# Kernel tuning notes

Hardware: AMD Instinct MI355X
Metric: run time of the kernel (lower is better)

Reference implementation:

```python
import jax, jax.numpy as jnp
import numpy as np

N, E, F, ED, L = 50000, 800000, 64, 16, 2
EPS_BN = 1e-5


def setup_inputs() -> dict:
    key = jax.random.key(0)
    ks = jax.random.split(key, 8)
    s = 0.05
    return {
        "x": jax.random.normal(ks[0], (N, F), jnp.float32),
        "edge_index": jax.random.randint(ks[1], (2, E), 0, N),
        "edge_attr": jax.random.normal(ks[2], (E, ED), jnp.float32),
        # per-layer stacked params (L layers)
        "We": jax.random.normal(ks[3], (L, ED, F), jnp.float32) * s,
        "be": jnp.zeros((L, F), jnp.float32),
        "Wpre": jax.random.normal(ks[4], (L, 2 * F, F), jnp.float32) * s,
        "bpre": jnp.zeros((L, F), jnp.float32),
        "Wpost": jax.random.normal(ks[5], (L, 7 * F, F), jnp.float32) * s,
        "bpost": jnp.zeros((L, F), jnp.float32),
        "Wlin": jax.random.normal(ks[6], (L, F, F), jnp.float32) * s,
        "blin": jnp.zeros((L, F), jnp.float32),
        "gamma": jnp.ones((L, F), jnp.float32),
        "beta": jnp.zeros((L, F), jnp.float32),
    }


def _layer(x, src, dst, edge_attr, We, be, Wpre, bpre, Wpost, bpost, Wlin, blin, gamma, beta):
    # message: edge encoder + pre-MLP on cat(x_j, e)   [E, F]
    e = edge_attr @ We + be
    h = jnp.concatenate([x[src], e], axis=-1) @ Wpre + bpre
    # multi-aggregator segment reduce to target nodes (index = dst)
    cnt = jax.ops.segment_sum(jnp.ones(h.shape[0], h.dtype), dst, num_segments=N)
    safe_cnt = jnp.maximum(cnt, 1.0)
    mean = jax.ops.segment_sum(h, dst, num_segments=N) / safe_cnt[:, None]
    empty = (cnt == 0)[:, None]
    mn = jnp.where(empty, 0.0, jax.ops.segment_min(h, dst, num_segments=N))
    mx = jnp.where(empty, 0.0, jax.ops.segment_max(h, dst, num_segments=N))
    agg = jnp.concatenate([mean, mn, mx], axis=-1)  # [N, 3F]
    # scalers: identity, then amplification (deg=None => avg from bincount of degrees)
    deg_i = cnt.astype(jnp.int32)
    bc = jnp.bincount(deg_i, length=N).astype(h.dtype)
    avg_log = jnp.mean(jnp.log(bc + 1.0))
    amp = (jnp.log(safe_cnt + 1.0) / avg_log)[:, None]
    out = jnp.concatenate([agg, agg * amp], axis=-1)  # [N, 6F]
    # post-MLP on cat(x, aggregated), final linear
    out = jnp.concatenate([x, out], axis=-1) @ Wpost + bpost  # [N, F]
    out = out @ Wlin + blin
    # BatchNorm1d (batch stats, biased var) + ReLU
    mu = out.mean(axis=0)
    var = jnp.mean((out - mu) ** 2, axis=0)
    out = gamma * (out - mu) / jnp.sqrt(var + EPS_BN) + beta
    return jax.nn.relu(out)


def reference(x, edge_index, edge_attr, We, be, Wpre, bpre, Wpost, bpost, Wlin, blin, gamma, beta):
    src, dst = edge_index[0], edge_index[1]
    for l in range(L):
        x = _layer(x, src, dst, edge_attr, We[l], be[l], Wpre[l], bpre[l],
                   Wpost[l], bpost[l], Wlin[l], blin[l], gamma[l], beta[l])
    return x
```

## Files before the change

### kernel.cpp

```cpp
#include <hip/hip_runtime.h>
#include <math.h>

static constexpr int NN = 50000;
static constexpr long NE = 800000;
static constexpr int FF = 64;
static constexpr int EDIM = 16;
static constexpr int NLAYER = 2;
static constexpr float EPSBN = 1e-5f;
static constexpr int NGRP = NN / 16;
static constexpr int SCB = 512;
static constexpr int NSCB = (NN + SCB - 1) / SCB;

typedef __attribute__((ext_vector_type(8))) short short8v;
typedef __attribute__((ext_vector_type(4))) float f32x4;

#define MFMA16(a, b, c) __builtin_amdgcn_mfma_f32_16x16x32_bf16(a, b, c, 0, 0, 0)

__device__ __forceinline__ short f2bf(float f) {
    unsigned u = __float_as_uint(f);
    unsigned r = u + 0x7FFFu + ((u >> 16) & 1u);
    return (short)(r >> 16);
}
__device__ __forceinline__ float bf2f(unsigned short h) {
    return __uint_as_float(((unsigned)h) << 16);
}
__device__ __forceinline__ unsigned pk2(float lo, float hi) {
    return (unsigned)(unsigned short)f2bf(lo) | ((unsigned)(unsigned short)f2bf(hi) << 16);
}
__device__ __forceinline__ short8v pack8(const float* p) {
    const float4* q = (const float4*)p;
    float4 a = q[0], b = q[1];
    short8v v;
    v[0] = f2bf(a.x); v[1] = f2bf(a.y); v[2] = f2bf(a.z); v[3] = f2bf(a.w);
    v[4] = f2bf(b.x); v[5] = f2bf(b.y); v[6] = f2bf(b.z); v[7] = f2bf(b.w);
    return v;
}
__device__ __forceinline__ void pack8s(const float* p, short8v& hi, short8v& lo) {
    const float4* q = (const float4*)p;
    float4 a = q[0], b = q[1];
    float v[8] = {a.x, a.y, a.z, a.w, b.x, b.y, b.z, b.w};
#pragma unroll
    for (int j = 0; j < 8; ++j) {
        short h = f2bf(v[j]);
        hi[j] = h;
        lo[j] = f2bf(v[j] - bf2f((unsigned short)h));
    }
}
__device__ __forceinline__ void pack8fs(const float* v, short8v& hi, short8v& lo) {
#pragma unroll
    for (int j = 0; j < 8; ++j) {
        short h = f2bf(v[j]);
        hi[j] = h;
        lo[j] = f2bf(v[j] - bf2f((unsigned short)h));
    }
}

__global__ void fold_kernel(const float* __restrict__ We, const float* __restrict__ be,
                            const float* __restrict__ Wpre, const float* __restrict__ bpre,
                            const float* __restrict__ Wpost, const float* __restrict__ bpost,
                            const float* __restrict__ Wlin, const float* __restrict__ blin,
                            float* __restrict__ Weff, float* __restrict__ beff,
                            float* __restrict__ Wc, float* __restrict__ cfold) {
    int l = blockIdx.x >> 4;
    int s = blockIdx.x & 15;
    int t = threadIdx.x;
    const float* We_l    = We    + l * EDIM * FF;
    const float* Wpre_e  = Wpre  + l * 2 * FF * FF + FF * FF;
    const float* Wpost_l = Wpost + l * 7 * FF * FF;
    const float* Wlin_l  = Wlin  + l * FF * FF;

    __shared__ float slin[FF * FF];
    __shared__ float spre[FF * FF];
    for (int i = t; i < FF * FF; i += blockDim.x) { slin[i] = Wlin_l[i]; spre[i] = Wpre_e[i]; }
    __syncthreads();

    for (int i = s * 256 + t; i < EDIM * FF; i += 16 * 256) {
        int j = i >> 6, f = i & 63;
        float a = 0.f;
        for (int k = 0; k < FF; ++k) a += We_l[j * FF + k] * spre[k * FF + f];
        Weff[l * EDIM * FF + i] = a;
    }
    for (int i = s * 256 + t; i < FF; i += 16 * 256) {
        float a = bpre[l * FF + i];
        for (int k = 0; k < FF; ++k) a += be[l * FF + k] * spre[k * FF + i];
        beff[l * FF + i] = a;
    }
    for (int i = s * 256 + t; i < 7 * FF * FF; i += 16 * 256) {
        int r = i >> 6, f = i & 63;
        float a = 0.f;
        for (int k = 0; k < FF; ++k) a += Wpost_l[r * FF + k] * slin[k * FF + f];
        Wc[l * 7 * FF * FF + i] = a;
    }
    for (int i = s * 256 + t; i < FF; i += 16 * 256) {
        float a = blin[l * FF + i];
        for (int k = 0; k < FF; ++k) a += bpost[l * FF + k] * slin[k * FF + i];
        cfold[l * FF + i] = a;
    }
}

__global__ void fragify_all(const float* __restrict__ Wpre, const float* __restrict__ Weff,
                            const float* __restrict__ Wc,
                            short* __restrict__ WpreF, short* __restrict__ WeffF,
                            short* __restrict__ WcFh, short* __restrict__ WcFl) {
    int b = blockIdx.x;
    int l = b / 17, r = b % 17;
    int t = threadIdx.x;
    const float* src; short* dh; short* dl = nullptr; int kc, Kreal;
    if (r < 2)      { src = Wpre + (size_t)l * 2 * FF * FF; dh = WpreF + l * 4096;  kc = r;     Kreal = 64; }
    else if (r < 3) { src = Weff + (size_t)l * EDIM * FF;   dh = WeffF + l * 2048;  kc = 0;     Kreal = 16; }
    else            { src = Wc   + (size_t)l * 7 * FF * FF; dh = WcFh + l * 28672;
                      dl = WcFl + l * 28672;                                        kc = r - 3; Kreal = 448; }
    int idx = kc * 256 + t;
    int lane = idx & 63, nt = (idx >> 6) & 3;
    int m = lane & 15, kh = lane >> 4;
    short8v hv, lv;
#pragma unroll
    for (int j = 0; j < 8; ++j) {
        int k = kc * 32 + kh * 8 + j;
        float val = (k < Kreal) ? src[k * FF + nt * 16 + m] : 0.f;
        short h = f2bf(val);
        hv[j] = h;
        lv[j] = f2bf(val - bf2f((unsigned short)h));
    }
    ((short8v*)dh)[idx] = hv;
    if (dl) ((short8v*)dl)[idx] = lv;
}


__global__ void build_zero(int* __restrict__ rowcnt, int* __restrict__ fill,
                           int* __restrict__ bc, float* __restrict__ avglog) {
    long i = (long)blockIdx.x * 256 + threadIdx.x;
    long stride = (long)gridDim.x * 256;
    for (long j = i; j < NN; j += stride) { rowcnt[j] = 0; fill[j] = 0; bc[j] = 0; }
    if (i == 0) avglog[0] = 0.f;
}

__global__ void hist_dst(const int* __restrict__ ei, int* __restrict__ rowcnt) {
    long e = (long)blockIdx.x * 256 + threadIdx.x;
    if (e < NE) atomicAdd(&rowcnt[ei[NE + e]], 1);
}

__global__ void scan_a(const int* __restrict__ rowcnt, int* __restrict__ part) {
    __shared__ int red[SCB];
    int t = threadIdx.x;
    int i = blockIdx.x * SCB + t;
    red[t] = (i < NN) ? rowcnt[i] : 0;
    __syncthreads();
    for (int o = SCB / 2; o > 0; o >>= 1) {
        if (t < o) red[t] += red[t + o];
        __syncthreads();
    }
    if (t == 0) part[blockIdx.x] = red[0];
}

__global__ void scan_b(int* __restrict__ part, int* __restrict__ rowptr) {
    __shared__ int s[128];
    int t = threadIdx.x;
    int v = (t < NSCB) ? part[t] : 0;
    s[t] = v;
    __syncthreads();
    for (int o = 1; o < 128; o <<= 1) {
        int u = (t >= o) ? s[t - o] : 0;
        __syncthreads();
        s[t] += u;
        __syncthreads();
    }
    if (t < NSCB) part[t] = s[t] - v;
    if (t == 127) rowptr[NN] = s[127];
}

__global__ void scan_c(const int* __restrict__ rowcnt, const int* __restrict__ part,
                       int* __restrict__ rowptr) {
    __shared__ int s[SCB];
    int t = threadIdx.x;
    int i = blockIdx.x * SCB + t;
    int v = (i < NN) ? rowcnt[i] : 0;
    s[t] = v;
    __syncthreads();
    for (int o = 1; o < SCB; o <<= 1) {
        int u = (t >= o) ? s[t - o] : 0;
        __syncthreads();
        s[t] += u;
        __syncthreads();
    }
    if (i < NN) rowptr[i] = part[blockIdx.x] + s[t] - v;
}

__global__ void scatter2(const int* __restrict__ ei, const float* __restrict__ attr,
                         const int* __restrict__ rowptr, int* __restrict__ fill,
                         int* __restrict__ srcp, short* __restrict__ attrb) {
    long e = (long)blockIdx.x * 256 + threadIdx.x;
    if (e >= NE) return;
    int d = ei[NE + e];
    int p = rowptr[d] + atomicAdd(&fill[d], 1);
    srcp[p] = ei[e];
    const float4* a4 = (const float4*)(attr + e * EDIM);
    float4 A = a4[0], B = a4[1], C = a4[2], D = a4[3];
    uint4 w0, w1;
    w0.x = pk2(A.x, A.y); w0.y = pk2(A.z, A.w); w0.z = pk2(B.x, B.y); w0.w = pk2(B.z, B.w);
    w1.x = pk2(C.x, C.y); w1.y = pk2(C.z, C.w); w1.z = pk2(D.x, D.y); w1.w = pk2(D.z, D.w);
    uint4* dst = (uint4*)(attrb + (long)p * EDIM);
    dst[0] = w0; dst[1] = w1;
}

__global__ void degbc2(const int* __restrict__ rowcnt, int* __restrict__ bc) {
    __shared__ int h[256];
    int t = threadIdx.x;
    h[t] = 0;
    __syncthreads();
    for (long n = (long)blockIdx.x * 256 + t; n < NN; n += (long)gridDim.x * 256) {
        int d = rowcnt[n];
        if (d < 256) {
            atomicAdd(&h[d], 1);
        } else {
            if (d >= NN) d = NN - 1;
            atomicAdd(&bc[d], 1);
        }
    }
    __syncthreads();
    int v = h[t];
    if (v) atomicAdd(&bc[t], v);
}

__global__ void avglog_kernel(const int* __restrict__ bc, float* __restrict__ total) {
    float s = 0.f;
    for (long i = (long)blockIdx.x * 256 + threadIdx.x; i < NN; i += (long)gridDim.x * 256)
        s += logf((float)bc[i] + 1.f);
    for (int o = 32; o; o >>= 1) s += __shfl_down(s, o, 64);
    __shared__ float wsum[4];
    int lane = threadIdx.x & 63, wid = threadIdx.x >> 6;
    if (lane == 0) wsum[wid] = s;
    __syncthreads();
    if (threadIdx.x == 0) atomicAdd(total, wsum[0] + wsum[1] + wsum[2] + wsum[3]);
}

__global__ void amp_kernel(const int* __restrict__ cnt, const float* __restrict__ total,
                           float* __restrict__ amp) {
    long n = (long)blockIdx.x * 256 + threadIdx.x;
    if (n < NN) {
        float avg = total[0] / (float)NN;
        float sc = fmaxf((float)cnt[n], 1.f);
        amp[n] = logf(sc + 1.f) / avg;
    }
}


__global__ __launch_bounds__(256) void xp_mfma(const float* __restrict__ xin,
                                               const short* __restrict__ WF,
                                               short* __restrict__ xpb,
                                               float* __restrict__ bnsum,
                                               float* __restrict__ bnsum2) {
    int t = threadIdx.x;
    if (blockIdx.x == 0 && t < FF) { bnsum[t] = 0.f; bnsum2[t] = 0.f; }
    int g = blockIdx.x * 4 + (t >> 6);
    if (g >= NGRP) return;
    int lane = t & 63, m = lane & 15, kh = lane >> 4;
    const float* xr = xin + (long)(g * 16 + m) * FF;
    short8v a0 = pack8(xr + kh * 8);
    short8v a1 = pack8(xr + 32 + kh * 8);
    const short8v* BF = (const short8v*)WF;
    f32x4 acc[4];
#pragma unroll
    for (int nt = 0; nt < 4; ++nt) {
        f32x4 z = {0.f, 0.f, 0.f, 0.f};
        z = MFMA16(a0, BF[(0 * 4 + nt) * 64 + lane], z);
        z = MFMA16(a1, BF[(1 * 4 + nt) * 64 + lane], z);
        acc[nt] = z;
    }
#pragma unroll
    for (int nt = 0; nt < 4; ++nt)
#pragma unroll
        for (int r = 0; r < 4; ++r) {
            long node = g * 16 + kh * 4 + r;
            xpb[node * FF + nt * 16 + m] = f2bf(acc[nt][r]);
        }
}

__global__ __launch_bounds__(256) void ep_mfma(const short* __restrict__ attrb,
                                               const short* __restrict__ WF,
                                               const float* __restrict__ beff_l,
                                               short* __restrict__ epc, long elo) {
    int t = threadIdx.x;
    int g = blockIdx.x * 4 + (t >> 6);
    int lane = t & 63, m = lane & 15, kh = lane >> 4;
    long p0 = elo + (long)g * 16;
    short8v a;
    if (kh < 2) {
        a = *(const short8v*)(attrb + (p0 + m) * EDIM + kh * 8);
    } else {
#pragma unroll
        for (int j = 0; j < 8; ++j) a[j] = 0;
    }
    const short8v* BF = (const short8v*)WF;
    float bfv[4];
#pragma unroll
    for (int nt = 0; nt < 4; ++nt) bfv[nt] = beff_l[nt * 16 + m];
    f32x4 acc[4];
#pragma unroll
    for (int nt = 0; nt < 4; ++nt) {
        f32x4 z = {0.f, 0.f, 0.f, 0.f};
        acc[nt] = MFMA16(a, BF[nt * 64 + lane], z);
    }
#pragma unroll
    for (int nt = 0; nt < 4; ++nt)
#pragma unroll
        for (int r = 0; r < 4; ++r) {
            long rel = (long)g * 16 + kh * 4 + r;
            epc[rel * FF + nt * 16 + m] = f2bf(acc[nt][r] + bfv[nt]);
        }
}

__global__ __launch_bounds__(256) void agg_merge(
    const int* __restrict__ rowptr, const int* __restrict__ srcp,
    const short* __restrict__ xpb, const short* __restrict__ epc,
    long elo, long ehi, int first,
    float* __restrict__ sumb, float* __restrict__ mnb, float* __restrict__ mxb) {
    int t = threadIdx.x;
    int n = blockIdx.x * 4 + (t >> 6);
    if (n >= NN) return;
    int lane = t & 63;
    long r0 = rowptr[n], r1 = rowptr[n + 1];
    long lo = r0 > elo ? r0 : elo;
    long hi = r1 < ehi ? r1 : ehi;
    const float INF = __builtin_huge_valf();
    float sm = 0.f, mn = INF, mx = -INF;
    if (!first && lo >= hi) return;
    const unsigned short* xu = (const unsigned short*)xpb;
    const unsigned short* eu = (const unsigned short*)epc;
    for (long base = lo; base < hi; base += 64) {
        int cnt = (int)(((hi - base) < 64) ? (hi - base) : 64);
        int sv = srcp[base + (lane < cnt ? lane : cnt - 1)];
        long eb = base - elo;
        int j = 0;
        for (; j + 4 <= cnt; j += 4) {
            int s0 = __shfl(sv, j + 0), s1 = __shfl(sv, j + 1);
            int s2 = __shfl(sv, j + 2), s3 = __shfl(sv, j + 3);
            float x0 = bf2f(xu[(long)s0 * FF + lane]);
            float x1 = bf2f(xu[(long)s1 * FF + lane]);
            float x2 = bf2f(xu[(long)s2 * FF + lane]);
            float x3 = bf2f(xu[(long)s3 * FF + lane]);
            float e0 = bf2f(eu[(eb + j + 0) * FF + lane]);
            float e1 = bf2f(eu[(eb + j + 1) * FF + lane]);
            float e2 = bf2f(eu[(eb + j + 2) * FF + lane]);
            float e3 = bf2f(eu[(eb + j + 3) * FF + lane]);
            float h0 = x0 + e0, h1 = x1 + e1, h2 = x2 + e2, h3 = x3 + e3;
            sm += (h0 + h1) + (h2 + h3);
            mn = fminf(mn, fminf(fminf(h0, h1), fminf(h2, h3)));
            mx = fmaxf(mx, fmaxf(fmaxf(h0, h1), fmaxf(h2, h3)));
        }
        for (; j < cnt; ++j) {
            int s0 = __shfl(sv, j);
            float h = bf2f(xu[(long)s0 * FF + lane]) + bf2f(eu[(eb + j) * FF + lane]);
            sm += h;
            mn = fminf(mn, h);
            mx = fmaxf(mx, h);
        }
    }
    long o = (long)n * FF + lane;
    if (first) {
        sumb[o] = sm; mnb[o] = mn; mxb[o] = mx;
    } else {
        sumb[o] += sm;
        mnb[o] = fminf(mnb[o], mn);
        mxb[o] = fmaxf(mxb[o], mx);
    }
}

__global__ __launch_bounds__(256) void node_mfma(
    const float* __restrict__ xin, const float* __restrict__ sumb,
    const float* __restrict__ mnb, const float* __restrict__ mxb,
    const int* __restrict__ rowcnt, const float* __restrict__ amp,
    const short* __restrict__ WFh, const short* __restrict__ WFl,
    const float* __restrict__ cfold_l,
    float* __restrict__ out_pre, float* __restrict__ bnsum, float* __restrict__ bnsum2) {
    __shared__ float sS[FF], sQ[FF];
    int t = threadIdx.x;
    if (t < FF) { sS[t] = 0.f; sQ[t] = 0.f; }
    __syncthreads();
    int g = blockIdx.x * 4 + (t >> 6);
    bool act = (g < NGRP);
    int lane = t & 63, m = lane & 15, kh = lane >> 4;
    if (act) {
        long n = g * 16 + m;
        int deg = rowcnt[n];
        float inv = 1.f / fmaxf((float)deg, 1.f);
        bool has = (deg > 0);
        float av = amp[n];
        const float* xr = xin + n * FF;
        float vme[16], vmn[16], vmx[16], sc16[16];
        {
            const float4* s4a = (const float4*)(sumb + n * FF + kh * 8);
            const float4* s4b = (const float4*)(sumb + n * FF + 32 + kh * 8);
            float4 a = s4a[0], b = s4a[1], c = s4b[0], d = s4b[1];
            vme[0]=a.x*inv; vme[1]=a.y*inv; vme[2]=a.z*inv; vme[3]=a.w*inv;
            vme[4]=b.x*inv; vme[5]=b.y*inv; vme[6]=b.z*inv; vme[7]=b.w*inv;
            vme[8]=c.x*inv; vme[9]=c.y*inv; vme[10]=c.z*inv; vme[11]=c.w*inv;
            vme[12]=d.x*inv; vme[13]=d.y*inv; vme[14]=d.z*inv; vme[15]=d.w*inv;
        }
        {
            const float4* s4a = (const float4*)(mnb + n * FF + kh * 8);
            const float4* s4b = (const float4*)(mnb + n * FF + 32 + kh * 8);
            float4 a = s4a[0], b = s4a[1], c = s4b[0], d = s4b[1];
            vmn[0]=has?a.x:0.f; vmn[1]=has?a.y:0.f; vmn[2]=has?a.z:0.f; vmn[3]=has?a.w:0.f;
            vmn[4]=has?b.x:0.f; vmn[5]=has?b.y:0.f; vmn[6]=has?b.z:0.f; vmn[7]=has?b.w:0.f;
            vmn[8]=has?c.x:0.f; vmn[9]=has?c.y:0.f; vmn[10]=has?c.z:0.f; vmn[11]=has?c.w:0.f;
            vmn[12]=has?d.x:0.f; vmn[13]=has?d.y:0.f; vmn[14]=has?d.z:0.f; vmn[15]=has?d.w:0.f;
        }
        {
            const float4* s4a = (const float4*)(mxb + n * FF + kh * 8);
            const float4* s4b = (const float4*)(mxb + n * FF + 32 + kh * 8);
            float4 a = s4a[0], b = s4a[1], c = s4b[0], d = s4b[1];
            vmx[0]=has?a.x:0.f; vmx[1]=has?a.y:0.f; vmx[2]=has?a.z:0.f; vmx[3]=has?a.w:0.f;
            vmx[4]=has?b.x:0.f; vmx[5]=has?b.y:0.f; vmx[6]=has?b.z:0.f; vmx[7]=has?b.w:0.f;
            vmx[8]=has?c.x:0.f; vmx[9]=has?c.y:0.f; vmx[10]=has?c.z:0.f; vmx[11]=has?c.w:0.f;
            vmx[12]=has?d.x:0.f; vmx[13]=has?d.y:0.f; vmx[14]=has?d.z:0.f; vmx[15]=has?d.w:0.f;
        }
        const short8v* BH = (const short8v*)WFh;
        const short8v* BL = (const short8v*)WFl;
        f32x4 acc[4];
#pragma unroll
        for (int nt = 0; nt < 4; ++nt) { f32x4 z = {0.f,0.f,0.f,0.f}; acc[nt] = z; }
        short8v hv, lv;
#define DO_KC3(kc) { \
        _Pragma("unroll") for (int nt = 0; nt < 4; ++nt) { \
            acc[nt] = MFMA16(hv, BH[((kc) * 4 + nt) * 64 + lane], acc[nt]); \
            acc[nt] = MFMA16(lv, BH[((kc) * 4 + nt) * 64 + lane], acc[nt]); \
            acc[nt] = MFMA16(hv, BL[((kc) * 4 + nt) * 64 + lane], acc[nt]); } }
        pack8s(xr + kh * 8, hv, lv);        DO_KC3(0)
        pack8s(xr + 32 + kh * 8, hv, lv);   DO_KC3(1)
        pack8fs(vme + 0, hv, lv);           DO_KC3(2)
        pack8fs(vme + 8, hv, lv);           DO_KC3(3)
        pack8fs(vmn + 0, hv, lv);           DO_KC3(4)
        pack8fs(vmn + 8, hv, lv);           DO_KC3(5)
        pack8fs(vmx + 0, hv, lv);           DO_KC3(6)
        pack8fs(vmx + 8, hv, lv);           DO_KC3(7)
#pragma unroll
        for (int j = 0; j < 16; ++j) sc16[j] = vme[j] * av;
        pack8fs(sc16 + 0, hv, lv);          DO_KC3(8)
        pack8fs(sc16 + 8, hv, lv);          DO_KC3(9)
#pragma unroll
        for (int j = 0; j < 16; ++j) sc16[j] = vmn[j] * av;
        pack8fs(sc16 + 0, hv, lv);          DO_KC3(10)
        pack8fs(sc16 + 8, hv, lv);          DO_KC3(11)
#pragma unroll
        for (int j = 0; j < 16; ++j) sc16[j] = vmx[j] * av;
        pack8fs(sc16 + 0, hv, lv);          DO_KC3(12)
        pack8fs(sc16 + 8, hv, lv);          DO_KC3(13)
#undef DO_KC3
        float cfv[4];
#pragma unroll
        for (int nt = 0; nt < 4; ++nt) cfv[nt] = cfold_l[nt * 16 + m];
#pragma unroll
        for (int nt = 0; nt < 4; ++nt) {
            float ps = 0.f, pq = 0.f;
#pragma unroll
            for (int r = 0; r < 4; ++r) {
                float v = acc[nt][r] + cfv[nt];
                out_pre[(long)(g * 16 + kh * 4 + r) * FF + nt * 16 + m] = v;
                ps += v;
                pq += v * v;
            }
            atomicAdd(&sS[nt * 16 + m], ps);
            atomicAdd(&sQ[nt * 16 + m], pq);
        }
    }
    __syncthreads();
    if (t < FF) {
        atomicAdd(&bnsum[t], sS[t]);
        atomicAdd(&bnsum2[t], sQ[t]);
    }
}

__global__ void bn_apply2(const float* __restrict__ out_pre,
                          const float* __restrict__ bnsum, const float* __restrict__ bnsum2,
                          const float* __restrict__ gamma_l, const float* __restrict__ beta_l,
                          float* __restrict__ xout) {
    int f = threadIdx.x & 63;
    float mu = bnsum[f] / (float)NN;
    float var = bnsum2[f] / (float)NN - mu * mu;
    var = fmaxf(var, 0.f);
    float s = gamma_l[f] * rsqrtf(var + EPSBN);
    float o = beta_l[f] - mu * s;
    long i = (long)blockIdx.x * 256 + threadIdx.x;
    long stride = (long)gridDim.x * 256;
    for (long j = i; j < (long)NN * FF; j += stride) {
        xout[j] = fmaxf(fmaf(out_pre[j], s, o), 0.f);
    }
}

extern "C" void kernel_launch(void* const* d_in, const int* in_sizes, int n_in,
                              void* d_out, int out_size, void* d_ws, size_t ws_size,
                              hipStream_t stream) {
    const float* x0    = (const float*)d_in[0];
    const int*   ei    = (const int*)d_in[1];
    const float* attr  = (const float*)d_in[2];
    const float* We    = (const float*)d_in[3];
    const float* be    = (const float*)d_in[4];
    const float* Wpre  = (const float*)d_in[5];
    const float* bpre  = (const float*)d_in[6];
    const float* Wpost = (const float*)d_in[7];
    const float* bpost = (const float*)d_in[8];
    const float* Wlin  = (const float*)d_in[9];
    const float* blin  = (const float*)d_in[10];
    const float* gamma = (const float*)d_in[11];
    const float* beta  = (const float*)d_in[12];
    float* out = (float*)d_out;

    char* ws = (char*)d_ws;
    size_t off = 0;
    auto carve = [&](size_t bytes) -> void* {
        void* p = ws + off;
        off += (bytes + 255) & ~(size_t)255;
        return p;
    };
    const size_t NFb = (size_t)NN * FF * 4;
    float*    Weff   = (float*)carve(2 * EDIM * FF * 4);
    float*    beff   = (float*)carve(2 * FF * 4);
    float*    Wc     = (float*)carve(2 * 7 * FF * FF * 4);
    float*    cfold  = (float*)carve(2 * FF * 4);
    short*    WpreF  = (short*)carve(2 * 4096 * 2);
    short*    WeffF  = (short*)carve(2 * 2048 * 2);
    short*    WcFh   = (short*)carve(2 * 28672 * 2);
    short*    WcFl   = (short*)carve(2 * 28672 * 2);
    int*      srcp   = (int*)carve(NE * 4);
    short*    attrb  = (short*)carve((size_t)NE * EDIM * 2);
    int*      rowptr = (int*)carve((NN + 1) * 4);
    int*      rowcnt = (int*)carve(NN * 4);
    int*      fill   = (int*)carve(NN * 4);
    int*      bc     = (int*)carve(NN * 4);
    float*    amp    = (float*)carve(NN * 4);
    int*      part   = (int*)carve(NSCB * 4);
    short*    xpb    = (short*)carve((size_t)NN * FF * 2);
    float*    sumb   = (float*)carve(NFb);
    float*    mnb    = (float*)carve(NFb);
    float*    mxb    = (float*)carve(NFb);
    float*    xbuf   = (float*)carve(NFb);
    float*    bnsum  = (float*)carve(FF * 4);
    float*    bnsum2 = (float*)carve(FF * 4);
    float*    avglog = (float*)carve(4);
    size_t left = (ws_size > off) ? ws_size - off : 0;
    long ech = (left >= (size_t)NE * FF * 2 + 512) ? NE : NE / 2;
    short*    epc    = (short*)carve((size_t)ech * FF * 2);
    float*    out_pre = (float*)epc;

    const int EB = (int)((NE + 255) / 256);

    build_zero<<<196, 256, 0, stream>>>(rowcnt, fill, bc, avglog);
    hist_dst<<<EB, 256, 0, stream>>>(ei, rowcnt);
    scan_a<<<NSCB, SCB, 0, stream>>>(rowcnt, part);
    scan_b<<<1, 128, 0, stream>>>(part, rowptr);
    scan_c<<<NSCB, SCB, 0, stream>>>(rowcnt, part, rowptr);
    scatter2<<<EB, 256, 0, stream>>>(ei, attr, rowptr, fill, srcp, attrb);
    degbc2<<<196, 256, 0, stream>>>(rowcnt, bc);
    avglog_kernel<<<128, 256, 0, stream>>>(bc, avglog);
    amp_kernel<<<196, 256, 0, stream>>>(rowcnt, avglog, amp);
    fold_kernel<<<32, 256, 0, stream>>>(We, be, Wpre, bpre, Wpost, bpost, Wlin, blin,
                                        Weff, beff, Wc, cfold);
    fragify_all<<<34, 256, 0, stream>>>(Wpre, Weff, Wc, WpreF, WeffF, WcFh, WcFl);

    for (int l = 0; l < NLAYER; ++l) {
        const float* xin = (l == 0) ? x0 : xbuf;
        float* xout = (l == NLAYER - 1) ? out : xbuf;

        xp_mfma<<<(NGRP + 3) / 4, 256, 0, stream>>>(xin, WpreF + l * 4096, xpb, bnsum, bnsum2);
        for (long elo = 0; elo < NE; elo += ech) {
            ep_mfma<<<(int)(ech / 64), 256, 0, stream>>>(attrb, WeffF + l * 2048,
                                                         beff + l * FF, epc, elo);
            agg_merge<<<12500, 256, 0, stream>>>(rowptr, srcp, xpb, epc, elo, elo + ech,
                                                 (elo == 0) ? 1 : 0, sumb, mnb, mxb);
        }
        node_mfma<<<(NGRP + 3) / 4, 256, 0, stream>>>(xin, sumb, mnb, mxb, rowcnt, amp,
                                                      WcFh + l * 28672, WcFl + l * 28672,
                                                      cfold + l * FF,
                                                      out_pre, bnsum, bnsum2);
        bn_apply2<<<4096, 256, 0, stream>>>(out_pre, bnsum, bnsum2,
                                            gamma + l * FF, beta + l * FF, xout);
    }
}
```

Measured before the change: 375.8 us.

## Split CSR scatter into permutation pass and gather, unroll aggregation by 8

Result: no change. 377.0 us (+0.3%).

```diff
diff --git a/kernel.cpp b/kernel.cpp
--- a/kernel.cpp
+++ b/kernel.cpp
@@ -186,20 +186,28 @@
     if (i < NN) rowptr[i] = part[blockIdx.x] + s[t] - v;
 }
 
-__global__ void scatter2(const int* __restrict__ ei, const float* __restrict__ attr,
-                         const int* __restrict__ rowptr, int* __restrict__ fill,
-                         int* __restrict__ srcp, short* __restrict__ attrb) {
+__global__ void scatter_perm(const int* __restrict__ ei, const int* __restrict__ rowptr,
+                             int* __restrict__ fill, int2* __restrict__ srcperm) {
     long e = (long)blockIdx.x * 256 + threadIdx.x;
     if (e >= NE) return;
     int d = ei[NE + e];
     int p = rowptr[d] + atomicAdd(&fill[d], 1);
-    srcp[p] = ei[e];
+    srcperm[p] = make_int2(ei[e], (int)e);
+}
+
+__global__ void gather_attr(const int2* __restrict__ srcperm, const float* __restrict__ attr,
+                            int* __restrict__ srcp, short* __restrict__ attrb) {
+    long p = (long)blockIdx.x * 256 + threadIdx.x;
+    if (p >= NE) return;
+    int2 sp = srcperm[p];
+    srcp[p] = sp.x;
+    long e = sp.y;
     const float4* a4 = (const float4*)(attr + e * EDIM);
     float4 A = a4[0], B = a4[1], C = a4[2], D = a4[3];
     uint4 w0, w1;
     w0.x = pk2(A.x, A.y); w0.y = pk2(A.z, A.w); w0.z = pk2(B.x, B.y); w0.w = pk2(B.z, B.w);
     w1.x = pk2(C.x, C.y); w1.y = pk2(C.z, C.w); w1.z = pk2(D.x, D.y); w1.w = pk2(D.z, D.w);
-    uint4* dst = (uint4*)(attrb + (long)p * EDIM);
+    uint4* dst = (uint4*)(attrb + p * EDIM);
     dst[0] = w0; dst[1] = w1;
 }
 
@@ -332,6 +340,35 @@
         int sv = srcp[base + (lane < cnt ? lane : cnt - 1)];
         long eb = base - elo;
         int j = 0;
+        for (; j + 8 <= cnt; j += 8) {
+            int s0 = __shfl(sv, j + 0), s1 = __shfl(sv, j + 1);
+            int s2 = __shfl(sv, j + 2), s3 = __shfl(sv, j + 3);
+            int s4 = __shfl(sv, j + 4), s5 = __shfl(sv, j + 5);
+            int s6 = __shfl(sv, j + 6), s7 = __shfl(sv, j + 7);
+            float x0 = bf2f(xu[(long)s0 * FF + lane]);
+            float x1 = bf2f(xu[(long)s1 * FF + lane]);
+            float x2 = bf2f(xu[(long)s2 * FF + lane]);
+            float x3 = bf2f(xu[(long)s3 * FF + lane]);
+            float x4 = bf2f(xu[(long)s4 * FF + lane]);
+            float x5 = bf2f(xu[(long)s5 * FF + lane]);
+            float x6 = bf2f(xu[(long)s6 * FF + lane]);
+            float x7 = bf2f(xu[(long)s7 * FF + lane]);
+            float e0 = bf2f(eu[(eb + j + 0) * FF + lane]);
+            float e1 = bf2f(eu[(eb + j + 1) * FF + lane]);
+            float e2 = bf2f(eu[(eb + j + 2) * FF + lane]);
+            float e3 = bf2f(eu[(eb + j + 3) * FF + lane]);
+            float e4 = bf2f(eu[(eb + j + 4) * FF + lane]);
+            float e5 = bf2f(eu[(eb + j + 5) * FF + lane]);
+            float e6 = bf2f(eu[(eb + j + 6) * FF + lane]);
+            float e7 = bf2f(eu[(eb + j + 7) * FF + lane]);
+            float h0 = x0 + e0, h1 = x1 + e1, h2 = x2 + e2, h3 = x3 + e3;
+            float h4 = x4 + e4, h5 = x5 + e5, h6 = x6 + e6, h7 = x7 + e7;
+            sm += ((h0 + h1) + (h2 + h3)) + ((h4 + h5) + (h6 + h7));
+            mn = fminf(mn, fminf(fminf(fminf(h0, h1), fminf(h2, h3)),
+                                 fminf(fminf(h4, h5), fminf(h6, h7))));
+            mx = fmaxf(mx, fmaxf(fmaxf(fmaxf(h0, h1), fmaxf(h2, h3)),
+                                 fmaxf(fmaxf(h4, h5), fmaxf(h6, h7))));
+        }
         for (; j + 4 <= cnt; j += 4) {
             int s0 = __shfl(sv, j + 0), s1 = __shfl(sv, j + 1);
             int s2 = __shfl(sv, j + 2), s3 = __shfl(sv, j + 3);
@@ -542,6 +579,7 @@
     long ech = (left >= (size_t)NE * FF * 2 + 512) ? NE : NE / 2;
     short*    epc    = (short*)carve((size_t)ech * FF * 2);
     float*    out_pre = (float*)epc;
+    int2*     srcperm = (int2*)xbuf;
 
     const int EB = (int)((NE + 255) / 256);
 
@@ -550,7 +588,8 @@
     scan_a<<<NSCB, SCB, 0, stream>>>(rowcnt, part);
     scan_b<<<1, 128, 0, stream>>>(part, rowptr);
     scan_c<<<NSCB, SCB, 0, stream>>>(rowcnt, part, rowptr);
-    scatter2<<<EB, 256, 0, stream>>>(ei, attr, rowptr, fill, srcp, attrb);
+    scatter_perm<<<EB, 256, 0, stream>>>(ei, rowptr, fill, srcperm);
+    gather_attr<<<EB, 256, 0, stream>>>(srcperm, attr, srcp, attrb);
     degbc2<<<196, 256, 0, stream>>>(rowcnt, bc);
     avglog_kernel<<<128, 256, 0, stream>>>(bc, avglog);
     amp_kernel<<<196, 256, 0, stream>>>(rowcnt, avglog, amp);
```
